# Kernel optimization log

Measured on AMD Instinct MI355X. Metric: run time of the kernel, lower is better.

Reference implementation:

```python
import jax, jax.numpy as jnp
import numpy as np

VOCAB, EMB, HID = 5000, 16, 32
B, T = 256, 2048


def setup_inputs() -> dict:
    key = jax.random.key(0)
    k1, k2, k3, k4, k5 = jax.random.split(key, 5)
    tokens = jax.random.randint(k1, (B, T), 0, VOCAB, dtype=jnp.int32)
    emb = jax.random.normal(k2, (VOCAB, EMB), dtype=jnp.float32) * 0.05
    Wk = jax.random.normal(k3, (EMB, 4 * HID), dtype=jnp.float32) * 0.1
    Wr = jax.random.normal(k4, (HID, 4 * HID), dtype=jnp.float32) * 0.1
    b = jax.random.normal(k5, (4 * HID,), dtype=jnp.float32) * 0.1
    return {"tokens": tokens, "emb": emb, "Wk": Wk, "Wr": Wr, "b": b}


def reference(tokens, emb, Wk, Wr, b):
    # Embedding lookup: [B, T, EMB]
    x = emb[tokens]
    # Mask: Keras Masking on tiled token values -> masked where token == 0.
    mask = (tokens != 0)  # [B, T] True = valid step
    # Precompute input projections for all timesteps: [B, T, 4H]
    zx = jnp.einsum('bte,eh->bth', x, Wk) + b
    zx_t = jnp.swapaxes(zx, 0, 1)        # [T, B, 4H]
    mask_t = jnp.swapaxes(mask, 0, 1)    # [T, B]

    def step(carry, inp):
        h, c = carry
        z_x, m = inp
        z = z_x + h @ Wr                      # [B, 4H]
        i, f, g, o = jnp.split(z, 4, axis=-1) # Keras gate order i,f,g,o
        i = jax.nn.sigmoid(i)
        f = jax.nn.sigmoid(f)
        g = jnp.tanh(g)
        o = jax.nn.sigmoid(o)
        c_new = f * c + i * g
        h_new = o * jnp.tanh(c_new)
        m = m[:, None]
        # Keras masked RNN: masked steps carry forward previous state/output
        h = jnp.where(m, h_new, h)
        c = jnp.where(m, c_new, c)
        return (h, c), h

    h0 = jnp.zeros((tokens.shape[0], HID), dtype=zx.dtype)
    c0 = jnp.zeros((tokens.shape[0], HID), dtype=zx.dtype)
    _, hs = jax.lax.scan(step, (h0, c0), (zx_t, mask_t))
    return jnp.swapaxes(hs, 0, 1)  # [B, T, HID]
```

## Files before the change

### kernel.cpp

```cpp
#include <hip/hip_runtime.h>

#define G    128
#define HID  32
#define EMB  16
#define BB   256
#define TT   2048
#define VOC  5000

typedef float v2f __attribute__((ext_vector_type(2)));
typedef __attribute__((ext_vector_type(8))) short short8;
typedef __attribute__((ext_vector_type(4))) float f32x4;

__device__ __forceinline__ float bf2f(unsigned short u) {
    return __uint_as_float(((unsigned)u) << 16);
}
__device__ __forceinline__ unsigned short f2bf(float f) {
    unsigned x = __float_as_uint(f);
    return (unsigned short)((x + 0x7FFFu + ((x >> 16) & 1u)) >> 16);
}
__device__ __forceinline__ float sigm(float x) {
    const float e = __expf(-x);
    return __builtin_amdgcn_rcpf(1.f + e);
}
__device__ __forceinline__ float tanh_f(float x) {
    const float e = __expf(-2.f * x);
    return (1.f - e) * __builtin_amdgcn_rcpf(1.f + e);
}
__device__ __forceinline__ float rdlf(float v, int k) {
    return __int_as_float(__builtin_amdgcn_readlane(__float_as_int(v), k));
}
template <int CTRL>
__device__ __forceinline__ unsigned dppq_u(unsigned v) {
    return (unsigned)__builtin_amdgcn_update_dpp(0, (int)v, CTRL, 0xF, 0xF, true);
}
template <int CTRL>
__device__ __forceinline__ float dppq_f(float v) {
    return __uint_as_float(dppq_u<CTRL>(__float_as_uint(v)));
}
#define DPP_XOR1 0xB1
#define DPP_XOR2 0x4E

__device__ __host__ __forceinline__ int col_a(int l) {
    return (l >> 1) + 32 * (l & 1);
}

__global__ void detect_kernel(const unsigned int* __restrict__ bias_w,
                              int* __restrict__ flag) {
    if (threadIdx.x == 0 && blockIdx.x == 0) {
        bool evens_zero = true, anybig = false;
        for (int i = 0; i < 64; ++i) {
            const unsigned u  = bias_w[i];
            const unsigned lo = u & 0xFFFFu;
            const float vlo = __uint_as_float(lo << 16);
            const float vhi = __uint_as_float(u & 0xFFFF0000u);
            if (lo != 0u) evens_zero = false;
            if (!(fabsf(vlo) < 1e6f) || !(fabsf(vhi) < 1e6f)) anybig = true;
        }
        *flag = (evens_zero || anybig) ? 1 : 0;
    }
}

__global__ __launch_bounds__(64) void zk_kernel(
    const void* __restrict__ emb, const void* __restrict__ Wk,
    const void* __restrict__ bias, float* __restrict__ ZK,
    const int* __restrict__ flag)
{
    const int l = threadIdx.x;
    const int v = blockIdx.x;
    const bool f32 = flag[0] != 0;
    const int ca = col_a(l), cb = ca + 64;

    float x[EMB], wa[EMB], wb[EMB], ba, bb;
    if (f32) {
        const float* E = (const float*)emb + (size_t)v * EMB;
        const float* W = (const float*)Wk;
        const float* B = (const float*)bias;
#pragma unroll
        for (int e = 0; e < EMB; ++e) {
            x[e]  = E[e];
            wa[e] = W[e * G + ca];
            wb[e] = W[e * G + cb];
        }
        ba = B[ca]; bb = B[cb];
    } else {
        const unsigned short* E = (const unsigned short*)emb + (size_t)v * EMB;
        const unsigned short* W = (const unsigned short*)Wk;
        const unsigned short* B = (const unsigned short*)bias;
#pragma unroll
        for (int e = 0; e < EMB; ++e) {
            x[e]  = bf2f(E[e]);
            wa[e] = bf2f(W[e * G + ca]);
            wb[e] = bf2f(W[e * G + cb]);
        }
        ba = bf2f(B[ca]); bb = bf2f(B[cb]);
    }
    float za = ba, zb = bb;
#pragma unroll
    for (int e = 0; e < EMB; ++e) {
        za = fmaf(x[e], wa[e], za);
        zb = fmaf(x[e], wb[e], zb);
    }
    ZK[(size_t)v * G + 2 * l]     = za;
    ZK[(size_t)v * G + 2 * l + 1] = zb;
}

template <bool F32OUT>
__device__ __forceinline__ void scan_zk_loop(
    const int* __restrict__ trow, const float* __restrict__ ZK,
    void* __restrict__ orow, const short8 (&Bf)[8], int lane)
{
    const bool  h0  = (lane & 1) == 0;
    const float zsc = h0 ? 2.f : 1.f, gm = h0 ? 2.f : 1.f, ga = h0 ? -1.f : 0.f;
    const int   oj  = lane >> 1;
    const int   g4  = (lane >> 4) & 3;
    const bool  u_odd = (lane >> 1) & 1;
    int badr[4];
#pragma unroll
    for (int q = 0; q < 4; ++q) badr[q] = 64 * (lane >> 4) + 16 * q;

    const f32x4 zc = {0.f, 0.f, 0.f, 0.f};
    float h = 0.f, c = 0.f;

    int tcur[16], tnxt[16];
#pragma unroll
    for (int p = 0; p < 16; ++p) tcur[p] = trow[p];
#pragma unroll
    for (int p = 0; p < 16; ++p) tnxt[p] = trow[16 + p];

    v2f pz[4];
#pragma unroll
    for (int d = 0; d < 4; ++d)
        pz[d] = *(const v2f*)(ZK + (size_t)tcur[d] * G + 2 * lane);

    for (int cc = 0; cc < TT / 16; ++cc) {
        const int base = cc * 16;
#pragma unroll
        for (int u = 0; u < 16; ++u) {
            const int t = base + u;
            const v2f z = pz[u & 3];
            {
                const int ptok = (u + 4 < 16) ? tcur[u + 4] : tnxt[u + 4 - 16];
                pz[u & 3] = *(const v2f*)(ZK + (size_t)ptok * G + 2 * lane);
            }

            const unsigned rh  = __float_as_uint(h) + 0x8000u;
            const unsigned prt = dppq_u<DPP_XOR2>(rh);
            const unsigned plo = u_odd ? prt : rh;
            const unsigned phi = u_odd ? rh : prt;
            const unsigned pair = __builtin_amdgcn_perm(phi, plo, 0x07060302u);
            union { unsigned u4[4]; short8 s8; } au;
#pragma unroll
            for (int q = 0; q < 4; ++q)
                au.u4[q] = (unsigned)__builtin_amdgcn_ds_bpermute(badr[q], (int)pair);
            const short8 Af = au.s8;

            f32x4 d0 = __builtin_amdgcn_mfma_f32_16x16x32_bf16(Af, Bf[0], zc, 0, 0, 0);
            f32x4 d1 = __builtin_amdgcn_mfma_f32_16x16x32_bf16(Af, Bf[1], zc, 0, 0, 0);
            f32x4 d2 = __builtin_amdgcn_mfma_f32_16x16x32_bf16(Af, Bf[2], zc, 0, 0, 0);
            f32x4 d3 = __builtin_amdgcn_mfma_f32_16x16x32_bf16(Af, Bf[3], zc, 0, 0, 0);
            f32x4 d4 = __builtin_amdgcn_mfma_f32_16x16x32_bf16(Af, Bf[4], zc, 0, 0, 0);
            f32x4 d5 = __builtin_amdgcn_mfma_f32_16x16x32_bf16(Af, Bf[5], zc, 0, 0, 0);
            f32x4 d6 = __builtin_amdgcn_mfma_f32_16x16x32_bf16(Af, Bf[6], zc, 0, 0, 0);
            f32x4 d7 = __builtin_amdgcn_mfma_f32_16x16x32_bf16(Af, Bf[7], zc, 0, 0, 0);

            const float mva = (g4 < 2) ? (g4 == 0 ? d0.x : d1.x)
                                       : (g4 == 2 ? d2.x : d3.x);
            const float mvb = (g4 < 2) ? (g4 == 0 ? d4.x : d5.x)
                                       : (g4 == 2 ? d6.x : d7.x);
            const float za = z.x + mva;
            const float zb = z.y + mvb;

            const float aa1 = sigm(za);
            const float s2  = sigm(zb * zsc);
            const float aa2 = fmaf(s2, gm, ga);
            const float x1  = dppq_f<DPP_XOR1>(aa1);
            const float x2  = dppq_f<DPP_XOR1>(aa2);
            const float iV = h0 ? aa1 : x1, fV = h0 ? x1 : aa1;
            const float gV = h0 ? aa2 : x2, oV = h0 ? x2 : aa2;
            const float cN = fmaf(fV, c, iV * gV);
            const float hN = oV * tanh_f(cN);
            const bool  m  = tcur[u] != 0;
            c = m ? cN : c;
            h = m ? hN : h;

            const int oi = t * HID + oj;
            if (F32OUT) __builtin_nontemporal_store(h, (float*)orow + oi);
            else        __builtin_nontemporal_store(f2bf(h), (unsigned short*)orow + oi);
        }
#pragma unroll
        for (int p = 0; p < 16; ++p) tcur[p] = tnxt[p];
        const int nb = (cc + 2) * 16;
        if (nb <= TT - 16) {
#pragma unroll
            for (int p = 0; p < 16; ++p) tnxt[p] = trow[nb + p];
        }
    }
}

__global__ __launch_bounds__(64) void scan_zk_kernel(
    const int* __restrict__ tokens, const float* __restrict__ ZK,
    const void* __restrict__ Wr, const void* __restrict__ bias,
    void* __restrict__ out, const int* __restrict__ flag)
{
    const int lane = threadIdx.x, b = blockIdx.x;
    const bool f32 = flag[0] != 0;

    short8 Bf[8];
    const int n  = lane & 15;
    const int k0 = (lane >> 4) * 8;
#pragma unroll
    for (int p = 0; p < 8; ++p) {
        const int ell = 16 * (p & 3) + n;
        const int col = (p < 4) ? col_a(ell) : (col_a(ell) + 64);
        short el[8];
        if (f32) {
            const float* W = (const float*)Wr;
#pragma unroll
            for (int j = 0; j < 8; ++j) el[j] = (short)f2bf(W[(k0 + j) * G + col]);
        } else {
            const unsigned short* W = (const unsigned short*)Wr;
#pragma unroll
            for (int j = 0; j < 8; ++j) el[j] = (short)W[(k0 + j) * G + col];
        }
        short8 s;
#pragma unroll
        for (int j = 0; j < 8; ++j) s[j] = el[j];
        Bf[p] = s;
    }

    const int* trow = tokens + (size_t)b * TT;
    if (f32) scan_zk_loop<true >(trow, ZK, (char*)out + (size_t)b * TT * HID * 4, Bf, lane);
    else     scan_zk_loop<false>(trow, ZK, (char*)out + (size_t)b * TT * HID * 2, Bf, lane);
}

template <bool F32>
__device__ __forceinline__ void row_load(const void* emb, int tok, uint4* r) {
    if (F32) { const uint4* p = (const uint4*)((const float*)emb + (size_t)tok*EMB);
               r[0]=p[0]; r[1]=p[1]; r[2]=p[2]; r[3]=p[3]; }
    else     { const uint4* p = (const uint4*)((const unsigned short*)emb + (size_t)tok*EMB);
               r[0]=p[0]; r[1]=p[1]; }
}
template <bool F32>
__device__ __forceinline__ void row_unpack(const uint4* r, float* x) {
    if (F32) {
        const unsigned w[16] = {r[0].x,r[0].y,r[0].z,r[0].w, r[1].x,r[1].y,r[1].z,r[1].w,
                                r[2].x,r[2].y,r[2].z,r[2].w, r[3].x,r[3].y,r[3].z,r[3].w};
#pragma unroll
        for (int e = 0; e < 16; ++e) x[e] = __uint_as_float(w[e]);
    } else {
        const unsigned w[8] = {r[0].x,r[0].y,r[0].z,r[0].w, r[1].x,r[1].y,r[1].z,r[1].w};
#pragma unroll
        for (int q = 0; q < 8; ++q) {
            x[2*q]   = __uint_as_float(w[q] << 16);
            x[2*q+1] = __uint_as_float(w[q] & 0xFFFF0000u);
        }
    }
}

template <bool F32>
__device__ __forceinline__ void scan_fused_loop(
    const int* __restrict__ trow, const void* __restrict__ emb, void* orow,
    const float (&wka)[EMB], const float (&wkb)[EMB],
    const float (&wra)[HID], const float (&wrb)[HID],
    float za0, float zb0, const int* tl, int lane)
{
    const bool  lo  = lane < HID;
    const float zsc = lo ? 2.f : 1.f, gm = lo ? 2.f : 1.f, ga = lo ? -1.f : 0.f;
    float h = 0.f, c = 0.f;
    uint4 praw[2][4];
    row_load<F32>(emb, trow[0], praw[0]);
    row_load<F32>(emb, trow[1], praw[1]);

    for (int tt = 0; tt < TT; tt += 2) {
#pragma unroll
        for (int u = 0; u < 2; ++u) {
            const int t = tt + u;
            float x[EMB];
            row_unpack<F32>(praw[u], x);
            int tn = t + 2; tn = tn > TT - 1 ? TT - 1 : tn;
            row_load<F32>(emb, tl[tn], praw[u]);
            float za = za0, zb = zb0;
#pragma unroll
            for (int e = 0; e < EMB; ++e) { za = fmaf(x[e], wka[e], za); zb = fmaf(x[e], wkb[e], zb); }
#pragma unroll
            for (int k = 0; k < HID; ++k) {
                const float hk = rdlf(h, k);
                za = fmaf(hk, wra[k], za);
                zb = fmaf(hk, wrb[k], zb);
            }
            const float a1 = sigm(za);
            const float s2 = sigm(zb * zsc);
            const float a2 = fmaf(s2, gm, ga);
            const float x1 = __shfl_xor(a1, 32);
            const float x2 = __shfl_xor(a2, 32);
            const float iV = lo ? a1 : x1, fV = lo ? x1 : a1;
            const float gV = lo ? a2 : x2, oV = lo ? x2 : a2;
            const float cN = fmaf(fV, c, iV * gV);
            const float hN = oV * tanh_f(cN);
            const bool  m  = tl[t] != 0;
            c = m ? cN : c;
            h = m ? hN : h;
            const int oi = t * HID + (lane & (HID - 1));
            if (F32) ((float*)orow)[oi] = h;
            else     ((unsigned short*)orow)[oi] = f2bf(h);
        }
    }
}

__global__ __launch_bounds__(64) void scan_fused_kernel(
    const int* __restrict__ tokens, const void* __restrict__ emb,
    const void* __restrict__ Wk, const void* __restrict__ Wr,
    const void* __restrict__ bias, void* __restrict__ out,
    const int* __restrict__ flag, int defmode)
{
    __shared__ int tl[TT];
    const int lane = threadIdx.x, b = blockIdx.x;
    const bool f32 = flag ? (flag[0] != 0) : (defmode != 0);
    const int* trow = tokens + (size_t)b * TT;
    for (int t = lane; t < TT; t += 64) tl[t] = trow[t];

    float wka[EMB], wkb[EMB], wra[HID], wrb[HID], za0, zb0;
    if (f32) {
        const float* WK = (const float*)Wk; const float* WR = (const float*)Wr;
        const float* B  = (const float*)bias;
#pragma unroll
        for (int e = 0; e < EMB; ++e) { wka[e] = WK[e*G + lane]; wkb[e] = WK[e*G + lane + 64]; }
#pragma unroll
        for (int k = 0; k < HID; ++k) { wra[k] = WR[k*G + lane]; wrb[k] = WR[k*G + lane + 64]; }
        za0 = B[lane]; zb0 = B[lane + 64];
    } else {
        const unsigned short* WK = (const unsigned short*)Wk;
        const unsigned short* WR = (const unsigned short*)Wr;
        const unsigned short* B  = (const unsigned short*)bias;
#pragma unroll
        for (int e = 0; e < EMB; ++e) { wka[e] = bf2f(WK[e*G + lane]); wkb[e] = bf2f(WK[e*G + lane + 64]); }
#pragma unroll
        for (int k = 0; k < HID; ++k) { wra[k] = bf2f(WR[k*G + lane]); wrb[k] = bf2f(WR[k*G + lane + 64]); }
        za0 = bf2f(B[lane]); zb0 = bf2f(B[lane + 64]);
    }
    __syncthreads();

    if (f32) scan_fused_loop<true >(trow, emb, (char*)out + (size_t)b*TT*HID*4,
                                    wka, wkb, wra, wrb, za0, zb0, tl, lane);
    else     scan_fused_loop<false>(trow, emb, (char*)out + (size_t)b*TT*HID*2,
                                    wka, wkb, wra, wrb, za0, zb0, tl, lane);
}

extern "C" void kernel_launch(void* const* d_in, const int* in_sizes, int n_in,
                              void* d_out, int out_size, void* d_ws, size_t ws_size,
                              hipStream_t stream) {
    const int*  tokens = (const int*)d_in[0];
    const void* emb    = d_in[1];
    const void* Wk     = d_in[2];
    const void* Wr     = d_in[3];
    const void* bias   = d_in[4];

    const size_t zk_off   = 256;
    const size_t zk_bytes = (size_t)VOC * G * sizeof(float);

    if (ws_size >= zk_off + zk_bytes) {
        int*   flag = (int*)d_ws;
        float* ZK   = (float*)((char*)d_ws + zk_off);
        detect_kernel<<<1, 64, 0, stream>>>((const unsigned int*)bias, flag);
        zk_kernel<<<VOC, 64, 0, stream>>>(emb, Wk, bias, ZK, flag);
        scan_zk_kernel<<<BB, 64, 0, stream>>>(tokens, ZK, Wr, bias, d_out, flag);
    } else if (ws_size >= 16) {
        int* flag = (int*)d_ws;
        detect_kernel<<<1, 64, 0, stream>>>((const unsigned int*)bias, flag);
        scan_fused_kernel<<<BB, 64, 0, stream>>>(tokens, emb, Wk, Wr, bias, d_out, flag, 1);
    } else {
        scan_fused_kernel<<<BB, 64, 0, stream>>>(tokens, emb, Wk, Wr, bias, d_out, nullptr, 1);
    }
}
```

Before: 533.0 us.

## Pack two sequences per wavefront with per-lane full gate computation

The recurrent scan now assigns two batch sequences to each 64-lane wavefront, one per 32-lane half. Each lane computes all four gates for its hidden unit, and the ZK table layout is changed to interleave gates so one 16-byte load serves them. This removes the DPP gate exchange and halves the MFMA work per sequence. In exchange, each lane evaluates more transcendentals per step and the launch uses half as many blocks.

```diff
diff --git a/kernel.cpp b/kernel.cpp
--- a/kernel.cpp
+++ b/kernel.cpp
@@ -8,6 +8,7 @@
 #define VOC  5000
 
 typedef float v2f __attribute__((ext_vector_type(2)));
+typedef float v4f __attribute__((ext_vector_type(4)));
 typedef __attribute__((ext_vector_type(8))) short short8;
 typedef __attribute__((ext_vector_type(4))) float f32x4;
 
@@ -29,20 +30,14 @@
 __device__ __forceinline__ float rdlf(float v, int k) {
     return __int_as_float(__builtin_amdgcn_readlane(__float_as_int(v), k));
 }
+__device__ __forceinline__ int rdli(int v, int k) {
+    return __builtin_amdgcn_readlane(v, k);
+}
 template <int CTRL>
 __device__ __forceinline__ unsigned dppq_u(unsigned v) {
     return (unsigned)__builtin_amdgcn_update_dpp(0, (int)v, CTRL, 0xF, 0xF, true);
 }
-template <int CTRL>
-__device__ __forceinline__ float dppq_f(float v) {
-    return __uint_as_float(dppq_u<CTRL>(__float_as_uint(v)));
-}
 #define DPP_XOR1 0xB1
-#define DPP_XOR2 0x4E
-
-__device__ __host__ __forceinline__ int col_a(int l) {
-    return (l >> 1) + 32 * (l & 1);
-}
 
 __global__ void detect_kernel(const unsigned int* __restrict__ bias_w,
                               int* __restrict__ flag) {
@@ -68,7 +63,9 @@
     const int l = threadIdx.x;
     const int v = blockIdx.x;
     const bool f32 = flag[0] != 0;
-    const int ca = col_a(l), cb = ca + 64;
+    const int e0 = 2 * l, e1 = 2 * l + 1;
+    const int c0 = 32 * (e0 & 3) + (e0 >> 2);
+    const int c1 = 32 * (e1 & 3) + (e1 >> 2);
 
     float x[EMB], wa[EMB], wb[EMB], ba, bb;
     if (f32) {
@@ -78,10 +75,10 @@
 #pragma unroll
         for (int e = 0; e < EMB; ++e) {
             x[e]  = E[e];
-            wa[e] = W[e * G + ca];
-            wb[e] = W[e * G + cb];
-        }
-        ba = B[ca]; bb = B[cb];
+            wa[e] = W[e * G + c0];
+            wb[e] = W[e * G + c1];
+        }
+        ba = B[c0]; bb = B[c1];
     } else {
         const unsigned short* E = (const unsigned short*)emb + (size_t)v * EMB;
         const unsigned short* W = (const unsigned short*)Wk;
@@ -89,10 +86,10 @@
 #pragma unroll
         for (int e = 0; e < EMB; ++e) {
             x[e]  = bf2f(E[e]);
-            wa[e] = bf2f(W[e * G + ca]);
-            wb[e] = bf2f(W[e * G + cb]);
-        }
-        ba = bf2f(B[ca]); bb = bf2f(B[cb]);
+            wa[e] = bf2f(W[e * G + c0]);
+            wb[e] = bf2f(W[e * G + c1]);
+        }
+        ba = bf2f(B[c0]); bb = bf2f(B[c1]);
     }
     float za = ba, zb = bb;
 #pragma unroll
@@ -100,137 +97,138 @@
         za = fmaf(x[e], wa[e], za);
         zb = fmaf(x[e], wb[e], zb);
     }
-    ZK[(size_t)v * G + 2 * l]     = za;
-    ZK[(size_t)v * G + 2 * l + 1] = zb;
+    v2f r; r.x = za; r.y = zb;
+    *(v2f*)(ZK + (size_t)v * G + e0) = r;
 }
 
 template <bool F32OUT>
-__device__ __forceinline__ void scan_zk_loop(
-    const int* __restrict__ trow, const float* __restrict__ ZK,
-    void* __restrict__ orow, const short8 (&Bf)[8], int lane)
-{
-    const bool  h0  = (lane & 1) == 0;
-    const float zsc = h0 ? 2.f : 1.f, gm = h0 ? 2.f : 1.f, ga = h0 ? -1.f : 0.f;
-    const int   oj  = lane >> 1;
-    const int   g4  = (lane >> 4) & 3;
-    const bool  u_odd = (lane >> 1) & 1;
+__device__ void scan2_loop(const int* __restrict__ trowme,
+                           const float* __restrict__ ZK,
+                           char* __restrict__ orowc,
+                           const short8 (&Bf)[8], int lane)
+{
+    const int  j    = lane & 31;
+    const bool r2   = (lane >> 4) & 1;
+    const bool odd  = lane & 1;
+    const int  zoff = 4 * j;
     int badr[4];
 #pragma unroll
-    for (int q = 0; q < 4; ++q) badr[q] = 64 * (lane >> 4) + 16 * q;
+    for (int q = 0; q < 4; ++q)
+        badr[q] = 4 * (32 * ((lane >> 3) & 1) + 8 * (lane >> 4) + 2 * q);
 
     const f32x4 zc = {0.f, 0.f, 0.f, 0.f};
     float h = 0.f, c = 0.f;
 
-    int tcur[16], tnxt[16];
-#pragma unroll
-    for (int p = 0; p < 16; ++p) tcur[p] = trow[p];
-#pragma unroll
-    for (int p = 0; p < 16; ++p) tnxt[p] = trow[16 + p];
-
-    v2f pz[4];
-#pragma unroll
-    for (int d = 0; d < 4; ++d)
-        pz[d] = *(const v2f*)(ZK + (size_t)tcur[d] * G + 2 * lane);
-
-    for (int cc = 0; cc < TT / 16; ++cc) {
-        const int base = cc * 16;
-#pragma unroll
-        for (int u = 0; u < 16; ++u) {
-            const int t = base + u;
-            const v2f z = pz[u & 3];
-            {
-                const int ptok = (u + 4 < 16) ? tcur[u + 4] : tnxt[u + 4 - 16];
-                pz[u & 3] = *(const v2f*)(ZK + (size_t)ptok * G + 2 * lane);
+    int vt0 = trowme[j];
+    int vt1 = trowme[32 + j];
+
+    v4f pz[4];
+#pragma unroll
+    for (int d = 0; d < 4; ++d) {
+        const int ta = rdli(vt0, d), tb = rdli(vt0, 32 + d);
+        const int tk = (lane & 32) ? tb : ta;
+        pz[d] = *(const v4f*)(ZK + (size_t)tk * G + zoff);
+    }
+
+    for (int cc = 0; cc < TT / 32; ++cc) {
+        const unsigned long long mw = __ballot(vt0 != 0);
+        for (int qq = 0; qq < 8; ++qq) {
+#pragma unroll
+            for (int u = 0; u < 4; ++u) {
+                const int q = qq * 4 + u;
+                const int t = cc * 32 + q;
+                const v4f z = pz[u];
+                {
+                    const int idx = q + 4;
+                    int ta, tb;
+                    if (idx < 32) { ta = rdli(vt0, idx); tb = rdli(vt0, idx + 32); }
+                    else          { ta = rdli(vt1, idx - 32); tb = rdli(vt1, idx); }
+                    const int tk = (lane & 32) ? tb : ta;
+                    pz[u] = *(const v4f*)(ZK + (size_t)tk * G + zoff);
+                }
+
+                const unsigned rh  = __float_as_uint(h) + 0x8000u;
+                const unsigned prt = dppq_u<DPP_XOR1>(rh);
+                const unsigned plo = odd ? prt : rh;
+                const unsigned phi = odd ? rh : prt;
+                const unsigned pair = __builtin_amdgcn_perm(phi, plo, 0x07060302u);
+                union { unsigned u4[4]; short8 s8; } au;
+#pragma unroll
+                for (int q2 = 0; q2 < 4; ++q2)
+                    au.u4[q2] = (unsigned)__builtin_amdgcn_ds_bpermute(badr[q2], (int)pair);
+                const short8 Af = au.s8;
+
+                f32x4 d0 = __builtin_amdgcn_mfma_f32_16x16x32_bf16(Af, Bf[0], zc, 0, 0, 0);
+                f32x4 d1 = __builtin_amdgcn_mfma_f32_16x16x32_bf16(Af, Bf[1], zc, 0, 0, 0);
+                f32x4 d2 = __builtin_amdgcn_mfma_f32_16x16x32_bf16(Af, Bf[2], zc, 0, 0, 0);
+                f32x4 d3 = __builtin_amdgcn_mfma_f32_16x16x32_bf16(Af, Bf[3], zc, 0, 0, 0);
+                f32x4 d4 = __builtin_amdgcn_mfma_f32_16x16x32_bf16(Af, Bf[4], zc, 0, 0, 0);
+                f32x4 d5 = __builtin_amdgcn_mfma_f32_16x16x32_bf16(Af, Bf[5], zc, 0, 0, 0);
+                f32x4 d6 = __builtin_amdgcn_mfma_f32_16x16x32_bf16(Af, Bf[6], zc, 0, 0, 0);
+                f32x4 d7 = __builtin_amdgcn_mfma_f32_16x16x32_bf16(Af, Bf[7], zc, 0, 0, 0);
+
+                const float zi = z.x + (r2 ? d4.x : d0.x);
+                const float zf = z.y + (r2 ? d5.x : d1.x);
+                const float zg = z.z + (r2 ? d6.x : d2.x);
+                const float zo = z.w + (r2 ? d7.x : d3.x);
+
+                const float iV = sigm(zi);
+                const float fV = sigm(zf);
+                const float s2 = sigm(2.f * zg);
+                const float gV = fmaf(s2, 2.f, -1.f);
+                const float oV = sigm(zo);
+                const float cN = fmaf(fV, c, iV * gV);
+                const float hN = oV * tanh_f(cN);
+
+                const int  sh = q + (lane & 32);
+                const bool m  = (mw >> sh) & 1ull;
+                c = m ? cN : c;
+                h = m ? hN : h;
+
+                const int oi = t * HID + j;
+                if (F32OUT) __builtin_nontemporal_store(h, (float*)orowc + oi);
+                else        __builtin_nontemporal_store(f2bf(h), (unsigned short*)orowc + oi);
             }
-
-            const unsigned rh  = __float_as_uint(h) + 0x8000u;
-            const unsigned prt = dppq_u<DPP_XOR2>(rh);
-            const unsigned plo = u_odd ? prt : rh;
-            const unsigned phi = u_odd ? rh : prt;
-            const unsigned pair = __builtin_amdgcn_perm(phi, plo, 0x07060302u);
-            union { unsigned u4[4]; short8 s8; } au;
-#pragma unroll
-            for (int q = 0; q < 4; ++q)
-                au.u4[q] = (unsigned)__builtin_amdgcn_ds_bpermute(badr[q], (int)pair);
-            const short8 Af = au.s8;
-
-            f32x4 d0 = __builtin_amdgcn_mfma_f32_16x16x32_bf16(Af, Bf[0], zc, 0, 0, 0);
-            f32x4 d1 = __builtin_amdgcn_mfma_f32_16x16x32_bf16(Af, Bf[1], zc, 0, 0, 0);
-            f32x4 d2 = __builtin_amdgcn_mfma_f32_16x16x32_bf16(Af, Bf[2], zc, 0, 0, 0);
-            f32x4 d3 = __builtin_amdgcn_mfma_f32_16x16x32_bf16(Af, Bf[3], zc, 0, 0, 0);
-            f32x4 d4 = __builtin_amdgcn_mfma_f32_16x16x32_bf16(Af, Bf[4], zc, 0, 0, 0);
-            f32x4 d5 = __builtin_amdgcn_mfma_f32_16x16x32_bf16(Af, Bf[5], zc, 0, 0, 0);
-            f32x4 d6 = __builtin_amdgcn_mfma_f32_16x16x32_bf16(Af, Bf[6], zc, 0, 0, 0);
-            f32x4 d7 = __builtin_amdgcn_mfma_f32_16x16x32_bf16(Af, Bf[7], zc, 0, 0, 0);
-
-            const float mva = (g4 < 2) ? (g4 == 0 ? d0.x : d1.x)
-                                       : (g4 == 2 ? d2.x : d3.x);
-            const float mvb = (g4 < 2) ? (g4 == 0 ? d4.x : d5.x)
-                                       : (g4 == 2 ? d6.x : d7.x);
-            const float za = z.x + mva;
-            const float zb = z.y + mvb;
-
-            const float aa1 = sigm(za);
-            const float s2  = sigm(zb * zsc);
-            const float aa2 = fmaf(s2, gm, ga);
-            const float x1  = dppq_f<DPP_XOR1>(aa1);
-            const float x2  = dppq_f<DPP_XOR1>(aa2);
-            const float iV = h0 ? aa1 : x1, fV = h0 ? x1 : aa1;
-            const float gV = h0 ? aa2 : x2, oV = h0 ? x2 : aa2;
-            const float cN = fmaf(fV, c, iV * gV);
-            const float hN = oV * tanh_f(cN);
-            const bool  m  = tcur[u] != 0;
-            c = m ? cN : c;
-            h = m ? hN : h;
-
-            const int oi = t * HID + oj;
-            if (F32OUT) __builtin_nontemporal_store(h, (float*)orow + oi);
-            else        __builtin_nontemporal_store(f2bf(h), (unsigned short*)orow + oi);
-        }
-#pragma unroll
-        for (int p = 0; p < 16; ++p) tcur[p] = tnxt[p];
-        const int nb = (cc + 2) * 16;
-        if (nb <= TT - 16) {
-#pragma unroll
-            for (int p = 0; p < 16; ++p) tnxt[p] = trow[nb + p];
-        }
-    }
-}
-
-__global__ __launch_bounds__(64) void scan_zk_kernel(
+        }
+        vt0 = vt1;
+        if (cc + 2 < TT / 32) vt1 = trowme[(cc + 2) * 32 + j];
+    }
+}
+
+__global__ __launch_bounds__(64) void scan_zk2_kernel(
     const int* __restrict__ tokens, const float* __restrict__ ZK,
     const void* __restrict__ Wr, const void* __restrict__ bias,
     void* __restrict__ out, const int* __restrict__ flag)
 {
     const int lane = threadIdx.x, b = blockIdx.x;
     const bool f32 = flag[0] != 0;
+    const int seq  = 2 * b + (lane >> 5);
 
     short8 Bf[8];
     const int n  = lane & 15;
     const int k0 = (lane >> 4) * 8;
 #pragma unroll
     for (int p = 0; p < 8; ++p) {
-        const int ell = 16 * (p & 3) + n;
-        const int col = (p < 4) ? col_a(ell) : (col_a(ell) + 64);
+        const int col = (p < 4) ? (32 * p + n) : (32 * (p - 4) + 16 + n);
         short el[8];
         if (f32) {
             const float* W = (const float*)Wr;
 #pragma unroll
-            for (int j = 0; j < 8; ++j) el[j] = (short)f2bf(W[(k0 + j) * G + col]);
+            for (int jj = 0; jj < 8; ++jj) el[jj] = (short)f2bf(W[(k0 + jj) * G + col]);
         } else {
             const unsigned short* W = (const unsigned short*)Wr;
 #pragma unroll
-            for (int j = 0; j < 8; ++j) el[j] = (short)W[(k0 + j) * G + col];
+            for (int jj = 0; jj < 8; ++jj) el[jj] = (short)W[(k0 + jj) * G + col];
         }
         short8 s;
 #pragma unroll
-        for (int j = 0; j < 8; ++j) s[j] = el[j];
+        for (int jj = 0; jj < 8; ++jj) s[jj] = el[jj];
         Bf[p] = s;
     }
 
-    const int* trow = tokens + (size_t)b * TT;
-    if (f32) scan_zk_loop<true >(trow, ZK, (char*)out + (size_t)b * TT * HID * 4, Bf, lane);
-    else     scan_zk_loop<false>(trow, ZK, (char*)out + (size_t)b * TT * HID * 2, Bf, lane);
+    const int* trowme = tokens + (size_t)seq * TT;
+    if (f32) scan2_loop<true >(trowme, ZK, (char*)out + (size_t)seq * TT * HID * 4, Bf, lane);
+    else     scan2_loop<false>(trowme, ZK, (char*)out + (size_t)seq * TT * HID * 2, Bf, lane);
 }
 
 template <bool F32>
@@ -363,7 +361,7 @@
         float* ZK   = (float*)((char*)d_ws + zk_off);
         detect_kernel<<<1, 64, 0, stream>>>((const unsigned int*)bias, flag);
         zk_kernel<<<VOC, 64, 0, stream>>>(emb, Wk, bias, ZK, flag);
-        scan_zk_kernel<<<BB, 64, 0, stream>>>(tokens, ZK, Wr, bias, d_out, flag);
+        scan_zk2_kernel<<<BB / 2, 64, 0, stream>>>(tokens, ZK, Wr, bias, d_out, flag);
     } else if (ws_size >= 16) {
         int* flag = (int*)d_ws;
         detect_kernel<<<1, 64, 0, stream>>>((const unsigned int*)bias, flag);
```

Result: slower. 588.5 us (+10.4%).
